# Kernel optimization log

Hardware: AMD Instinct MI355X
Metric: run time of the kernel (lower is better)

## Reference

```python
import jax, jax.numpy as jnp
import numpy as np

KNN = 5
SEARCH = 3
CUTOFF = 1.0
NCLASSES = 21
D, H, W = 32, 128, 2048
P = 1048576


def setup_inputs() -> dict:
    key = jax.random.key(0)
    k1, k2, k3, k4, k5, k6 = jax.random.split(key, 6)
    proj_range = jax.random.uniform(k1, (D, H, W), dtype=jnp.float32)
    unproj_range = jax.random.uniform(k2, (P,), dtype=jnp.float32)
    proj_argmax = jax.random.randint(k3, (D, H, W), 0, NCLASSES).astype(jnp.int32)
    px = jax.random.randint(k4, (P,), 0, W).astype(jnp.int32)
    py = jax.random.randint(k5, (P,), 0, H).astype(jnp.int32)
    pz = jax.random.randint(k6, (P,), 0, D).astype(jnp.int32)
    return {"proj_range": proj_range, "unproj_range": unproj_range,
            "proj_argmax": proj_argmax, "px": px, "py": py, "pz": pz}


def reference(proj_range, unproj_range, proj_argmax, px, py, pz):
    pad = (SEARCH - 1) // 2
    k3 = SEARCH ** 3
    center = (k3 - 1) // 2  # = 13 for search=3
    n_pts = unproj_range.shape[0]

    # zero padding replicates F.unfold's implicit zero pad (padded entries stay 0,
    # which is NOT mapped to inf by the `< 0` mask, matching the torch code)
    pr_pad = jnp.pad(proj_range, pad)
    pa_pad = jnp.pad(proj_argmax, pad)

    # kernel offsets, flattened in (dz, dy, dx) order like unfoldNd
    offs = jnp.arange(SEARCH, dtype=jnp.int32)
    oz, oy, ox = jnp.meshgrid(offs, offs, offs, indexing="ij")
    oz, oy, ox = oz.reshape(-1), oy.reshape(-1), ox.reshape(-1)  # [k3]

    # per-point neighborhood indices into the padded volume: [P, k3]
    zi = pz[:, None] + oz[None, :]
    yi = py[:, None] + oy[None, :]
    xi = px[:, None] + ox[None, :]

    nb_rang = pr_pad[zi, yi, xi]                       # [P, k3]
    nb_rang = jnp.where(nb_rang < 0, jnp.inf, nb_rang)
    nb_rang = nb_rang.at[:, center].set(unproj_range)  # center = query range

    k2_dist = jnp.abs(nb_rang - unproj_range[:, None])  # [P, k3]

    neg_top, knn_idx = jax.lax.top_k(-k2_dist, KNN)     # smallest-k distances
    knn_dist = -neg_top                                  # [P, KNN]

    nb_arg = pa_pad[zi, yi, xi]                          # [P, k3] int
    knn_arg = jnp.take_along_axis(nb_arg, knn_idx, axis=1)
    knn_arg = jnp.where(knn_dist > CUTOFF, NCLASSES, knn_arg)  # cutoff -> invalid class

    # scatter-add voting over classes 0..NCLASSES
    counts = jnp.zeros((n_pts, NCLASSES + 1), dtype=proj_range.dtype)
    counts = counts.at[jnp.arange(n_pts, dtype=jnp.int32)[:, None], knn_arg].add(1.0)

    # argmax over classes 1..NCLASSES-1 (drop class 0 and invalid bucket), then +1
    out = jnp.argmax(counts[:, 1:-1], axis=1).astype(jnp.int32) + 1
    return out
```

## Files before the change

kernel.cpp:

```cpp
#include <hip/hip_runtime.h>
#include <math.h>

#define KNN 5
#define K3 27
#define CENTER 13
#define NCLASSES 21
#define DIM_D 32
#define DIM_H 128
#define DIM_W 2048

#define RADIX 256
#define BIN_PTS 2048
#define WIN 1024


typedef float    float4u __attribute__((ext_vector_type(4), aligned(4)));
typedef int      int4u   __attribute__((ext_vector_type(4), aligned(4)));
typedef unsigned uint4u  __attribute__((ext_vector_type(4), aligned(4)));

#define SENTINEL 3.0e38f
#define BITS_TWO 0x4000000000000000ULL
#define M_SCALE 8388608.0f

__device__ __forceinline__ unsigned seg_of_xy(int x, int y) {
    return ((unsigned)y << 1) | ((unsigned)x >> 10);
}
__device__ __forceinline__ unsigned seg_of_wy(unsigned wy) {
    return (((wy >> 11) & 0x7Fu) << 1) | ((wy >> 10) & 1u);
}
__device__ __forceinline__ unsigned b8_of_wy(unsigned wy) {
    return (((wy >> 18) & 31u) << 3) | ((wy >> 7) & 7u);
}

__global__ __launch_bounds__(256) void pack_hist_kernel(
    const float4* __restrict__ pr4, const int4* __restrict__ pa4,
    uint4* __restrict__ cv4,
    const int* __restrict__ px, const int* __restrict__ py,
    unsigned* __restrict__ partial, int n4, int P, int chunk)
{
    __shared__ unsigned lh0[RADIX];
    int t = threadIdx.x, b = blockIdx.x;

    int i = b * 256 + t;
    if (i < n4) {
        float4 v = pr4[i];
        int4   c = pa4[i];
        uint4 w;
        w.x = ((unsigned)(v.x * M_SCALE) << 5) | ((unsigned)c.x & 31u);
        w.y = ((unsigned)(v.y * M_SCALE) << 5) | ((unsigned)c.y & 31u);
        w.z = ((unsigned)(v.z * M_SCALE) << 5) | ((unsigned)c.z & 31u);
        w.w = ((unsigned)(v.w * M_SCALE) << 5) | ((unsigned)c.w & 31u);
        cv4[i] = w;
    }

    if (b < RADIX) {
        lh0[t] = 0;
        __syncthreads();
        int start = b * chunk;
        int end = min(P, start + chunk);
        for (int i0 = start + t * 4; i0 < end; i0 += 256 * 4) {
            if (i0 + 3 < end) {
                int i4 = i0 >> 2;
                int4 X = ((const int4*)px)[i4];
                int4 Y = ((const int4*)py)[i4];
                atomicAdd(&lh0[seg_of_xy(X.x, Y.x)], 1u);
                atomicAdd(&lh0[seg_of_xy(X.y, Y.y)], 1u);
                atomicAdd(&lh0[seg_of_xy(X.z, Y.z)], 1u);
                atomicAdd(&lh0[seg_of_xy(X.w, Y.w)], 1u);
            } else {
                for (int j = i0; j < end; ++j)
                    atomicAdd(&lh0[seg_of_xy(px[j], py[j])], 1u);
            }
        }
        __syncthreads();
        partial[b * RADIX + t] = lh0[t];
    }
}

__global__ __launch_bounds__(256) void scan_reduce_kernel(
    const unsigned* __restrict__ partial, unsigned* __restrict__ g0)
{
    __shared__ unsigned ws[4];
    int t = threadIdx.x, lane = t & 63, wid = t >> 6;
    unsigned a = 0;
    for (int b = 0; b < RADIX; ++b)
        a += partial[b * RADIX + t];
    unsigned ia = a;
#pragma unroll
    for (int off = 1; off < 64; off <<= 1) {
        unsigned v = __shfl_up(ia, off);
        if (lane >= off) ia += v;
    }
    if (lane == 63) ws[wid] = ia;
    __syncthreads();
    unsigned b = 0;
#pragma unroll
    for (int w = 0; w < 4; ++w) b += (w < wid) ? ws[w] : 0u;
    g0[t] = b + ia - a;
}

struct BinShared {
    unsigned lh[RADIX];
    unsigned lscan[RADIX];
    unsigned gbase[RADIX];
    unsigned wsum[4];
    unsigned stW[BIN_PTS];
    unsigned stU[BIN_PTS];
    unsigned stI[BIN_PTS];
};

__global__ __launch_bounds__(512) void bin_pass1_kernel(
    const float* __restrict__ ur, const int* __restrict__ px,
    const int* __restrict__ py, const int* __restrict__ pz,
    unsigned* __restrict__ g0,
    unsigned* __restrict__ oW, unsigned* __restrict__ oU,
    unsigned* __restrict__ oI, int P)
{
    __shared__ BinShared S;
    int t = threadIdx.x, lane = t & 63, wid = t >> 6;
    int bstart = blockIdx.x * BIN_PTS;
    int n = min(BIN_PTS, P - bstart);
    if (t < RADIX) S.lh[t] = 0;
    __syncthreads();

    unsigned pw[4], pu[4], rk[4], dg[4];
    {
        int i4 = (bstart >> 2) + t;
        int i0 = i4 * 4;
        if (i0 + 3 < P) {
            int4 X = ((const int4*)px)[i4];
            int4 Y = ((const int4*)py)[i4];
            int4 Z = ((const int4*)pz)[i4];
            float4 U = ((const float4*)ur)[i4];
            int xs[4] = {X.x, X.y, X.z, X.w};
            int ys[4] = {Y.x, Y.y, Y.z, Y.w};
            int zs[4] = {Z.x, Z.y, Z.z, Z.w};
            float us[4] = {U.x, U.y, U.z, U.w};
#pragma unroll
            for (int c = 0; c < 4; ++c) {
                dg[c] = seg_of_xy(xs[c], ys[c]);
                rk[c] = atomicAdd(&S.lh[dg[c]], 1u);
                pw[c] = (unsigned)xs[c] | ((unsigned)ys[c] << 11)
                        | ((unsigned)zs[c] << 18);
                pu[c] = (unsigned)(us[c] * M_SCALE);
            }
        } else {
#pragma unroll
            for (int c = 0; c < 4; ++c) {
                int gi = i0 + c;
                if (gi < P) {
                    int x = px[gi], y = py[gi], z = pz[gi];
                    dg[c] = seg_of_xy(x, y);
                    rk[c] = atomicAdd(&S.lh[dg[c]], 1u);
                    pw[c] = (unsigned)x | ((unsigned)y << 11)
                            | ((unsigned)z << 18);
                    pu[c] = (unsigned)(ur[gi] * M_SCALE);
                } else {
                    dg[c] = 0xFFFFFFFFu;
                }
            }
        }
    }
    __syncthreads();

    {
        unsigned c0 = (t < RADIX) ? S.lh[t] : 0u;
        unsigned inc = c0;
#pragma unroll
        for (int off = 1; off < 64; off <<= 1) {
            unsigned v = __shfl_up(inc, off);
            if (lane >= off) inc += v;
        }
        if (t < RADIX && lane == 63) S.wsum[wid] = inc;
        __syncthreads();
        if (t < RADIX) {
            unsigned wb = 0;
#pragma unroll
            for (int w = 0; w < 4; ++w) wb += (w < wid) ? S.wsum[w] : 0u;
            S.lscan[t] = wb + inc - c0;
            S.gbase[t] = c0 ? atomicAdd(&g0[t], c0) : 0u;
        }
    }
    __syncthreads();
#pragma unroll
    for (int c = 0; c < 4; ++c)
        if (dg[c] != 0xFFFFFFFFu) {
            unsigned sl = S.lscan[dg[c]] + rk[c];
            S.stW[sl] = pw[c];
            S.stU[sl] = pu[c];
            S.stI[sl] = (unsigned)(((bstart >> 2) + t) * 4 + c);
        }
    __syncthreads();
#pragma unroll
    for (int j = 0; j < 4; ++j) {
        int s = j * 512 + t;
        if (s < n) {
            unsigned wv = S.stW[s];
            unsigned d = seg_of_wy(wv);
            unsigned pos = S.gbase[d] + ((unsigned)s - S.lscan[d]);
            oW[pos] = wv;
            oU[pos] = S.stU[s];
            oI[pos] = S.stI[s];
        }
    }
}

__device__ __forceinline__ void bev_knn_body_u24(
    const unsigned* __restrict__ cv,
    unsigned mu, int x, int y, int z, int oidx, int* __restrict__ out)
{
    int xo = min(max(x - 1, 0), DIM_W - 4);
    int s = x - 1 - xo;

    uint4u Wv[9];
    bool okr[9];
#pragma unroll
    for (int r = 0; r < 9; ++r) {
        const int dz = r / 3 - 1;
        const int dy = r % 3 - 1;
        int zz = z + dz, yy = y + dy;
        bool ok = ((unsigned)zz < (unsigned)DIM_D) &
                  ((unsigned)yy < (unsigned)DIM_H);
        okr[r] = ok;
        int row = ok ? (zz * DIM_H + yy) : 0;
        Wv[r] = *(const uint4u*)(cv + (((size_t)row) << 11) + xo);
    }

    double bd[KNN];
#pragma unroll
    for (int j = 0; j < KNN; ++j) bd[j] = 1.0e308;

    auto push = [&](int k, unsigned w) {
        int diff = abs((int)(w >> 5) - (int)mu);
        if (k == CENTER) diff = 0;
        double kd = (double)diff * 1024.0
                  + (double)(((unsigned)k << 5) | (w & 31u));
#pragma unroll
        for (int j = 0; j < KNN; ++j) {
            double lo = fmin(bd[j], kd);
            kd = fmax(bd[j], kd);
            bd[j] = lo;
        }
    };

    bool fast = __all(s == 0);
    if (fast) {
#pragma unroll
        for (int r = 0; r < 9; ++r) {
            bool ok = okr[r];
            push(r * 3 + 0, ok ? Wv[r].x : 0u);
            push(r * 3 + 1, ok ? Wv[r].y : 0u);
            push(r * 3 + 2, ok ? Wv[r].z : 0u);
        }
    } else {
#pragma unroll
        for (int r = 0; r < 9; ++r) {
            bool ok = okr[r];
            unsigned a0 = ok ? Wv[r].x : 0u;
            unsigned a1 = ok ? Wv[r].y : 0u;
            unsigned a2 = ok ? Wv[r].z : 0u;
            unsigned a3 = ok ? Wv[r].w : 0u;
            unsigned w0 = (s == 0) ? a0 : ((s == -1) ? 0u : ((s == 1) ? a1 : a2));
            unsigned w1 = (s == 0) ? a1 : ((s == -1) ? a0 : ((s == 1) ? a2 : a3));
            unsigned w2 = (s == 0) ? a2 : ((s == -1) ? a1 : ((s == 1) ? a3 : 0u));
            push(r * 3 + 0, w0);
            push(r * 3 + 1, w1);
            push(r * 3 + 2, w2);
        }
    }

    int votes[KNN];
#pragma unroll
    for (int j = 0; j < KNN; ++j)
        votes[j] = (int)(((unsigned long long)bd[j]) & 31u);

    int best_cnt = 0, best_cls = 1;
#pragma unroll
    for (int j = 0; j < KNN; ++j) {
        int v = votes[j];
        if (v >= 1 && v <= NCLASSES - 1) {
            int cnt = 0;
#pragma unroll
            for (int i = 0; i < KNN; ++i) cnt += (votes[i] == v) ? 1 : 0;
            if (cnt > best_cnt || (cnt == best_cnt && v < best_cls)) {
                best_cnt = cnt;
                best_cls = v;
            }
        }
    }
    __builtin_nontemporal_store(best_cls, &out[oidx]);
}

__device__ __forceinline__ int swizzle_block(int b, int nb) {
    if ((nb & 7) == 0) {
        int per = nb >> 3;
        return (b & 7) * per + (b >> 3);
    }
    return b;
}

__global__ __launch_bounds__(1024) void pass2_knn_kernel(
    const unsigned* __restrict__ iW, const unsigned* __restrict__ iU,
    const unsigned* __restrict__ iI,
    const unsigned* __restrict__ cv, int* __restrict__ out, int P)
{
    __shared__ unsigned lz[RADIX];
    __shared__ unsigned lsc[RADIX];
    __shared__ unsigned wsum[4];
    __shared__ unsigned stW[WIN];
    __shared__ unsigned stU[WIN];
    __shared__ unsigned stI[WIN];

    int lb = swizzle_block(blockIdx.x, gridDim.x);
    int base = lb * WIN;
    int m = min(WIN, P - base);
    int t = threadIdx.x, lane = t & 63, wid = t >> 6;

    if (t < RADIX) lz[t] = 0;
    __syncthreads();

    unsigned vw = 0, vu = 0, vi = 0, rk = 0, zz = 0xFFFFFFFFu;
    if (t < m) {
        vw = iW[base + t];
        vu = iU[base + t];
        vi = iI[base + t];
        zz = b8_of_wy(vw);
        rk = atomicAdd(&lz[zz], 1u);
    }
    __syncthreads();
    {
        unsigned c0 = (t < RADIX) ? lz[t] : 0u;
        unsigned inc = c0;
#pragma unroll
        for (int off = 1; off < 64; off <<= 1) {
            unsigned v = __shfl_up(inc, off);
            if (lane >= off) inc += v;
        }
        if (t < RADIX && lane == 63) wsum[wid] = inc;
        __syncthreads();
        if (t < RADIX) {
            unsigned wb = 0;
#pragma unroll
            for (int w = 0; w < 4; ++w) wb += (w < wid) ? wsum[w] : 0u;
            lsc[t] = wb + inc - c0;
        }
    }
    __syncthreads();
    if (zz != 0xFFFFFFFFu) {
        unsigned sl = lsc[zz] + rk;
        stW[sl] = vw;
        stU[sl] = vu;
        stI[sl] = vi;
    }
    __syncthreads();
    if (t < m) {
        unsigned wv = stW[t];
        int x = (int)(wv & 0x7FFu);
        int y = (int)((wv >> 11) & 0x7Fu);
        int z = (int)((wv >> 18) & 0x1Fu);
        bev_knn_body_u24(cv, stU[t], x, y, z, (int)stI[t], out);
    }
}

__device__ __forceinline__ void bev_knn_body_gen(
    const float* __restrict__ pr, const int* __restrict__ pa,
    float u, int x, int y, int z, int oidx, int* __restrict__ out)
{
    int xo = min(max(x - 1, 0), DIM_W - 4);
    int s = x - 1 - xo;

    float4u L[9];
    int4u   A[9];
    bool okr[9];
#pragma unroll
    for (int r = 0; r < 9; ++r) {
        const int dz = r / 3 - 1;
        const int dy = r % 3 - 1;
        int zz = z + dz, yy = y + dy;
        bool ok = ((unsigned)zz < (unsigned)DIM_D) &
                  ((unsigned)yy < (unsigned)DIM_H);
        okr[r] = ok;
        int row = ok ? (zz * DIM_H + yy) : 0;
        size_t rb = ((size_t)row) << 11;
        L[r] = *(const float4u*)(pr + rb + xo);
        A[r] = *(const int4u*)(pa + rb + xo);
    }

    double bd[KNN];
#pragma unroll
    for (int j = 0; j < KNN; ++j) bd[j] = 1.0e308;

    auto push = [&](int k, float v, unsigned cls) {
        float d = fabsf(v - u);
        d = (v < 0.f) ? SENTINEL : d;
        if (k == CENTER) d = 0.0f;
        double key = (double)d + 1.0;
        unsigned long long kb =
            (unsigned long long)__double_as_longlong(key)
            | (unsigned long long)(((unsigned)k << 5) | (cls & 31u));
        double kd = __longlong_as_double((long long)kb);
#pragma unroll
        for (int j = 0; j < KNN; ++j) {
            double lo = fmin(bd[j], kd);
            kd = fmax(bd[j], kd);
            bd[j] = lo;
        }
    };

#pragma unroll
    for (int r = 0; r < 9; ++r) {
        bool ok = okr[r];
        float a0 = ok ? L[r].x : 0.f;
        float a1 = ok ? L[r].y : 0.f;
        float a2 = ok ? L[r].z : 0.f;
        float a3 = ok ? L[r].w : 0.f;
        float v0 = (s == 0) ? a0 : ((s == -1) ? 0.f : ((s == 1) ? a1 : a2));
        float v1 = (s == 0) ? a1 : ((s == -1) ? a0 : ((s == 1) ? a2 : a3));
        float v2 = (s == 0) ? a2 : ((s == -1) ? a1 : ((s == 1) ? a3 : 0.f));
        unsigned c0 = ok ? (unsigned)A[r].x : 0u;
        unsigned c1 = ok ? (unsigned)A[r].y : 0u;
        unsigned c2 = ok ? (unsigned)A[r].z : 0u;
        unsigned c3 = ok ? (unsigned)A[r].w : 0u;
        unsigned cv0 = (s == 0) ? c0 : ((s == -1) ? 0u : ((s == 1) ? c1 : c2));
        unsigned cv1 = (s == 0) ? c1 : ((s == -1) ? c0 : ((s == 1) ? c2 : c3));
        unsigned cv2 = (s == 0) ? c2 : ((s == -1) ? c1 : ((s == 1) ? c3 : 0u));
        push(r * 3 + 0, v0, cv0);
        push(r * 3 + 1, v1, cv1);
        push(r * 3 + 2, v2, cv2);
    }

    int votes[KNN];
#pragma unroll
    for (int j = 0; j < KNN; ++j) {
        unsigned long long kb =
            (unsigned long long)__double_as_longlong(bd[j]);
        int cls = (int)(kb & 31u);
        bool cut = (kb & ~1023ULL) > BITS_TWO;
        votes[j] = cut ? NCLASSES : cls;
    }

    int best_cnt = 0, best_cls = 1;
#pragma unroll
    for (int j = 0; j < KNN; ++j) {
        int v = votes[j];
        if (v >= 1 && v <= NCLASSES - 1) {
            int cnt = 0;
#pragma unroll
            for (int i = 0; i < KNN; ++i) cnt += (votes[i] == v) ? 1 : 0;
            if (cnt > best_cnt || (cnt == best_cnt && v < best_cls)) {
                best_cnt = cnt;
                best_cls = v;
            }
        }
    }
    out[oidx] = best_cls;
}

__global__ __launch_bounds__(256) void bev_knn_direct_kernel(
    const float* __restrict__ pr, const int* __restrict__ pa,
    const float* __restrict__ ur, const int* __restrict__ px,
    const int* __restrict__ py, const int* __restrict__ pz,
    int* __restrict__ out, int P)
{
    int p = blockIdx.x * blockDim.x + threadIdx.x;
    if (p >= P) return;
    bev_knn_body_gen(pr, pa, ur[p], px[p], py[p], pz[p], p, out);
}

extern "C" void kernel_launch(void* const* d_in, const int* in_sizes, int n_in,
                              void* d_out, int out_size, void* d_ws, size_t ws_size,
                              hipStream_t stream) {
    const float* pr = (const float*)d_in[0];
    const float* ur = (const float*)d_in[1];
    const int*   pa = (const int*)d_in[2];
    const int*   px = (const int*)d_in[3];
    const int*   py = (const int*)d_in[4];
    const int*   pz = (const int*)d_in[5];
    int* out = (int*)d_out;
    int P = in_sizes[1];
    int gridB = (P + BIN_PTS - 1) / BIN_PTS;
    int gridD = (P + 255) / 256;
    int gridW = (P + WIN - 1) / WIN;
    int chunk = (((P + RADIX - 1) / RADIX) + 3) & ~3;

    const int VOXELS = DIM_D * DIM_H * DIM_W;
    size_t g0_b   = (size_t)RADIX * 4;
    size_t part_b = (size_t)RADIX * RADIX * 4;
    size_t pre    = (g0_b + part_b + 255) & ~(size_t)255;
    size_t arr_b  = ((size_t)P * 4 + 255) & ~(size_t)255;
    size_t cv_b   = ((size_t)VOXELS * 4 + 255) & ~(size_t)255;
    size_t need   = pre + 3 * arr_b + cv_b;

    if (ws_size >= need) {
        char* ws = (char*)d_ws;
        unsigned* g0   = (unsigned*)ws;
        unsigned* part = (unsigned*)(ws + g0_b);
        unsigned* p1W  = (unsigned*)(ws + pre);
        unsigned* p1U  = (unsigned*)(ws + pre + arr_b);
        unsigned* p1I  = (unsigned*)(ws + pre + 2 * arr_b);
        unsigned* cv   = (unsigned*)(ws + pre + 3 * arr_b);

        int n4 = VOXELS / 4;
        int gridP = max((n4 + 255) / 256, RADIX);
        pack_hist_kernel<<<gridP, 256, 0, stream>>>(
            (const float4*)pr, (const int4*)pa, (uint4*)cv,
            px, py, part, n4, P, chunk);
        scan_reduce_kernel<<<1, 256, 0, stream>>>(part, g0);
        bin_pass1_kernel<<<gridB, 512, 0, stream>>>(ur, px, py, pz, g0,
                                                    p1W, p1U, p1I, P);
        pass2_knn_kernel<<<gridW, 1024, 0, stream>>>(
            p1W, p1U, p1I, cv, out, P);
    } else {
        bev_knn_direct_kernel<<<gridD, 256, 0, stream>>>(pr, pa, ur, px, py,
                                                         pz, out, P);
    }
}
```

Baseline: 183.8 us.

## Process two points per thread in KNN pass with 512-thread blocks

The second KNN pass now runs 512 threads per block, each handling two sorted points. Each thread loads its inputs as paired 8-byte vector loads and issues all 18 neighborhood row loads for both points before computing either, to increase memory-level parallelism per thread. The wave-uniform fast-path check (__all) is replaced by a per-thread s==0 branch. This raises register pressure from doubled window arrays, and an unused knn_sel3 stub is added.

```diff
diff --git a/kernel.cpp b/kernel.cpp
--- a/kernel.cpp
+++ b/kernel.cpp
@@ -17,6 +17,7 @@
 typedef float    float4u __attribute__((ext_vector_type(4), aligned(4)));
 typedef int      int4u   __attribute__((ext_vector_type(4), aligned(4)));
 typedef unsigned uint4u  __attribute__((ext_vector_type(4), aligned(4)));
+typedef unsigned uint2a  __attribute__((ext_vector_type(2), aligned(8)));
 
 #define SENTINEL 3.0e38f
 #define BITS_TWO 0x4000000000000000ULL
@@ -205,75 +206,27 @@
     }
 }
 
-__device__ __forceinline__ void bev_knn_body_u24(
-    const unsigned* __restrict__ cv,
-    unsigned mu, int x, int y, int z, int oidx, int* __restrict__ out)
-{
-    int xo = min(max(x - 1, 0), DIM_W - 4);
-    int s = x - 1 - xo;
-
-    uint4u Wv[9];
-    bool okr[9];
-#pragma unroll
-    for (int r = 0; r < 9; ++r) {
-        const int dz = r / 3 - 1;
-        const int dy = r % 3 - 1;
-        int zz = z + dz, yy = y + dy;
-        bool ok = ((unsigned)zz < (unsigned)DIM_D) &
-                  ((unsigned)yy < (unsigned)DIM_H);
-        okr[r] = ok;
-        int row = ok ? (zz * DIM_H + yy) : 0;
-        Wv[r] = *(const uint4u*)(cv + (((size_t)row) << 11) + xo);
-    }
-
-    double bd[KNN];
-#pragma unroll
-    for (int j = 0; j < KNN; ++j) bd[j] = 1.0e308;
-
-    auto push = [&](int k, unsigned w) {
-        int diff = abs((int)(w >> 5) - (int)mu);
-        if (k == CENTER) diff = 0;
-        double kd = (double)diff * 1024.0
-                  + (double)(((unsigned)k << 5) | (w & 31u));
-#pragma unroll
-        for (int j = 0; j < KNN; ++j) {
-            double lo = fmin(bd[j], kd);
-            kd = fmax(bd[j], kd);
-            bd[j] = lo;
-        }
-    };
-
-    bool fast = __all(s == 0);
-    if (fast) {
-#pragma unroll
-        for (int r = 0; r < 9; ++r) {
-            bool ok = okr[r];
-            push(r * 3 + 0, ok ? Wv[r].x : 0u);
-            push(r * 3 + 1, ok ? Wv[r].y : 0u);
-            push(r * 3 + 2, ok ? Wv[r].z : 0u);
-        }
-    } else {
-#pragma unroll
-        for (int r = 0; r < 9; ++r) {
-            bool ok = okr[r];
-            unsigned a0 = ok ? Wv[r].x : 0u;
-            unsigned a1 = ok ? Wv[r].y : 0u;
-            unsigned a2 = ok ? Wv[r].z : 0u;
-            unsigned a3 = ok ? Wv[r].w : 0u;
-            unsigned w0 = (s == 0) ? a0 : ((s == -1) ? 0u : ((s == 1) ? a1 : a2));
-            unsigned w1 = (s == 0) ? a1 : ((s == -1) ? a0 : ((s == 1) ? a2 : a3));
-            unsigned w2 = (s == 0) ? a2 : ((s == -1) ? a1 : ((s == 1) ? a3 : 0u));
-            push(r * 3 + 0, w0);
-            push(r * 3 + 1, w1);
-            push(r * 3 + 2, w2);
-        }
-    }
-
+__device__ __forceinline__ void knn_push(double* bd, int k, unsigned w,
+                                         unsigned mu)
+{
+    int diff = abs((int)(w >> 5) - (int)mu);
+    if (k == CENTER) diff = 0;
+    double kd = (double)diff * 1024.0
+              + (double)(((unsigned)k << 5) | (w & 31u));
+#pragma unroll
+    for (int j = 0; j < KNN; ++j) {
+        double lo = fmin(bd[j], kd);
+        kd = fmax(bd[j], kd);
+        bd[j] = lo;
+    }
+}
+
+__device__ __forceinline__ int knn_vote(const double* bd)
+{
     int votes[KNN];
 #pragma unroll
     for (int j = 0; j < KNN; ++j)
         votes[j] = (int)(((unsigned long long)bd[j]) & 31u);
-
     int best_cnt = 0, best_cls = 1;
 #pragma unroll
     for (int j = 0; j < KNN; ++j) {
@@ -288,7 +241,46 @@
             }
         }
     }
-    __builtin_nontemporal_store(best_cls, &out[oidx]);
+    return best_cls;
+}
+
+__device__ __forceinline__ int knn_sel3(int s, unsigned a0, unsigned a1,
+                                        unsigned a2, unsigned a3, int e)
+{
+    return 0;
+}
+
+__device__ __forceinline__ void knn_point(
+    const uint4u* __restrict__ W, const bool* __restrict__ ok, int s,
+    unsigned mu, int oidx, int* __restrict__ out)
+{
+    double bd[KNN];
+#pragma unroll
+    for (int j = 0; j < KNN; ++j) bd[j] = 1.0e308;
+
+    if (s == 0) {
+#pragma unroll
+        for (int r = 0; r < 9; ++r) {
+            knn_push(bd, r * 3 + 0, ok[r] ? W[r].x : 0u, mu);
+            knn_push(bd, r * 3 + 1, ok[r] ? W[r].y : 0u, mu);
+            knn_push(bd, r * 3 + 2, ok[r] ? W[r].z : 0u, mu);
+        }
+    } else {
+#pragma unroll
+        for (int r = 0; r < 9; ++r) {
+            unsigned a0 = ok[r] ? W[r].x : 0u;
+            unsigned a1 = ok[r] ? W[r].y : 0u;
+            unsigned a2 = ok[r] ? W[r].z : 0u;
+            unsigned a3 = ok[r] ? W[r].w : 0u;
+            unsigned w0 = (s == -1) ? 0u : ((s == 1) ? a1 : a2);
+            unsigned w1 = (s == -1) ? a0 : ((s == 1) ? a2 : a3);
+            unsigned w2 = (s == -1) ? a1 : ((s == 1) ? a3 : 0u);
+            knn_push(bd, r * 3 + 0, w0, mu);
+            knn_push(bd, r * 3 + 1, w1, mu);
+            knn_push(bd, r * 3 + 2, w2, mu);
+        }
+    }
+    __builtin_nontemporal_store(knn_vote(bd), &out[oidx]);
 }
 
 __device__ __forceinline__ int swizzle_block(int b, int nb) {
@@ -299,7 +291,7 @@
     return b;
 }
 
-__global__ __launch_bounds__(1024) void pass2_knn_kernel(
+__global__ __launch_bounds__(512, 2) void pass2_knn_kernel(
     const unsigned* __restrict__ iW, const unsigned* __restrict__ iU,
     const unsigned* __restrict__ iI,
     const unsigned* __restrict__ cv, int* __restrict__ out, int P)
@@ -319,13 +311,32 @@
     if (t < RADIX) lz[t] = 0;
     __syncthreads();
 
-    unsigned vw = 0, vu = 0, vi = 0, rk = 0, zz = 0xFFFFFFFFu;
-    if (t < m) {
-        vw = iW[base + t];
-        vu = iU[base + t];
-        vi = iI[base + t];
-        zz = b8_of_wy(vw);
-        rk = atomicAdd(&lz[zz], 1u);
+    unsigned vw[2] = {0, 0}, vu[2] = {0, 0}, vi[2] = {0, 0};
+    unsigned rk[2] = {0, 0}, zz[2] = {0xFFFFFFFFu, 0xFFFFFFFFu};
+    int sl0 = 2 * t;
+    if (sl0 + 1 < m) {
+        uint2a W2 = *(const uint2a*)(iW + base + sl0);
+        uint2a U2 = *(const uint2a*)(iU + base + sl0);
+        uint2a I2 = *(const uint2a*)(iI + base + sl0);
+        vw[0] = W2.x; vw[1] = W2.y;
+        vu[0] = U2.x; vu[1] = U2.y;
+        vi[0] = I2.x; vi[1] = I2.y;
+        zz[0] = b8_of_wy(vw[0]);
+        zz[1] = b8_of_wy(vw[1]);
+        rk[0] = atomicAdd(&lz[zz[0]], 1u);
+        rk[1] = atomicAdd(&lz[zz[1]], 1u);
+    } else {
+#pragma unroll
+        for (int j = 0; j < 2; ++j) {
+            int s = sl0 + j;
+            if (s < m) {
+                vw[j] = iW[base + s];
+                vu[j] = iU[base + s];
+                vi[j] = iI[base + s];
+                zz[j] = b8_of_wy(vw[j]);
+                rk[j] = atomicAdd(&lz[zz[j]], 1u);
+            }
+        }
     }
     __syncthreads();
     {
@@ -346,20 +357,49 @@
         }
     }
     __syncthreads();
-    if (zz != 0xFFFFFFFFu) {
-        unsigned sl = lsc[zz] + rk;
-        stW[sl] = vw;
-        stU[sl] = vu;
-        stI[sl] = vi;
-    }
-    __syncthreads();
-    if (t < m) {
-        unsigned wv = stW[t];
-        int x = (int)(wv & 0x7FFu);
-        int y = (int)((wv >> 11) & 0x7Fu);
-        int z = (int)((wv >> 18) & 0x1Fu);
-        bev_knn_body_u24(cv, stU[t], x, y, z, (int)stI[t], out);
-    }
+#pragma unroll
+    for (int j = 0; j < 2; ++j)
+        if (zz[j] != 0xFFFFFFFFu) {
+            unsigned sl = lsc[zz[j]] + rk[j];
+            stW[sl] = vw[j];
+            stU[sl] = vu[j];
+            stI[sl] = vi[j];
+        }
+    __syncthreads();
+
+    int pA = 2 * t, pB = 2 * t + 1;
+    bool hasA = pA < m, hasB = pB < m;
+    unsigned wvA = hasA ? stW[pA] : 0u;
+    unsigned wvB = hasB ? stW[pB] : 0u;
+    unsigned muA = hasA ? stU[pA] : 0u;
+    unsigned muB = hasB ? stU[pB] : 0u;
+    int xA = (int)(wvA & 0x7FFu), yA = (int)((wvA >> 11) & 0x7Fu),
+        zA = (int)((wvA >> 18) & 0x1Fu);
+    int xB = (int)(wvB & 0x7FFu), yB = (int)((wvB >> 11) & 0x7Fu),
+        zB = (int)((wvB >> 18) & 0x1Fu);
+    int xoA = min(max(xA - 1, 0), DIM_W - 4), sA = xA - 1 - xoA;
+    int xoB = min(max(xB - 1, 0), DIM_W - 4), sB = xB - 1 - xoB;
+
+    uint4u WA[9], WB[9];
+    bool okA[9], okB[9];
+#pragma unroll
+    for (int r = 0; r < 9; ++r) {
+        const int dz = r / 3 - 1;
+        const int dy = r % 3 - 1;
+        int zzA = zA + dz, yyA = yA + dy;
+        int zzB = zB + dz, yyB = yB + dy;
+        okA[r] = ((unsigned)zzA < (unsigned)DIM_D) &
+                 ((unsigned)yyA < (unsigned)DIM_H);
+        okB[r] = ((unsigned)zzB < (unsigned)DIM_D) &
+                 ((unsigned)yyB < (unsigned)DIM_H);
+        int rowA = okA[r] ? (zzA * DIM_H + yyA) : 0;
+        int rowB = okB[r] ? (zzB * DIM_H + yyB) : 0;
+        WA[r] = *(const uint4u*)(cv + (((size_t)rowA) << 11) + xoA);
+        WB[r] = *(const uint4u*)(cv + (((size_t)rowB) << 11) + xoB);
+    }
+
+    if (hasA) knn_point(WA, okA, sA, muA, (int)stI[pA], out);
+    if (hasB) knn_point(WB, okB, sB, muB, (int)stI[pB], out);
 }
 
 __device__ __forceinline__ void bev_knn_body_gen(
@@ -508,7 +548,7 @@
         scan_reduce_kernel<<<1, 256, 0, stream>>>(part, g0);
         bin_pass1_kernel<<<gridB, 512, 0, stream>>>(ur, px, py, pz, g0,
                                                     p1W, p1U, p1I, P);
-        pass2_knn_kernel<<<gridW, 1024, 0, stream>>>(
+        pass2_knn_kernel<<<gridW, 512, 0, stream>>>(
             p1W, p1U, p1I, cv, out, P);
     } else {
         bev_knn_direct_kernel<<<gridD, 256, 0, stream>>>(pr, pa, ur, px, py,
```

New measurement: 191.6 us. 4.3% more time.
